# Optimization experiments

Measured on AMD Instinct MI355X. Metric: run time of the kernel, lower is better.

## Reference

```python
import jax, jax.numpy as jnp
import numpy as np

N, F, OUT = 8192, 256, 256


def setup_inputs() -> dict:
    key = jax.random.key(0)
    ks = jax.random.split(key, 8)
    s = 1.0 / np.sqrt(F)
    return {
        "features": jax.random.normal(ks[0], (N, F), jnp.float32),
        "key_features": jax.random.normal(ks[1], (N, F), jnp.float32),
        "adj_matrix": jax.random.uniform(ks[2], (N, N), jnp.float32),
        "W_d": jax.random.normal(ks[3], (2 * F, F), jnp.float32) * (1.0 / np.sqrt(2 * F)),
        "b_d": jnp.zeros((F,), jnp.float32),
        "W_o": jax.random.normal(ks[4], (F, OUT), jnp.float32) * s,
        "b_o": jnp.zeros((OUT,), jnp.float32),
        "W_a": jax.random.normal(ks[5], (F, F), jnp.float32) * s,
        "b_a": jnp.zeros((F,), jnp.float32),
        "W_ao": jax.random.normal(ks[6], (F, OUT), jnp.float32) * s,
        "b_ao": jnp.zeros((OUT,), jnp.float32),
    }


def reference(features, key_features, adj_matrix, W_d, b_d, W_o, b_o, W_a, b_a, W_ao, b_ao):
    n = features.shape[0]
    # masked softmax over rows; self-loop (diagonal) masked out
    neg = jnp.asarray(-1e9, adj_matrix.dtype)
    logits = adj_matrix * 5.0 + jnp.eye(n, dtype=adj_matrix.dtype) * neg
    a = jax.nn.softmax(logits, axis=-1)  # [N, N]
    # sum_j a_ij * concat(x_i, x_j) == concat(x_i * rowsum_i, (A @ X)_i)
    rowsum = jnp.sum(a, axis=-1, keepdims=True)  # == 1, kept for faithfulness
    agg = a @ features  # [N, F]
    neigh = jnp.concatenate([features * rowsum, agg], axis=-1)  # [N, 2F]
    neigh_distill = neigh @ W_d + b_d
    feature_updated = jnp.tanh((features - neigh_distill) @ W_o + b_o)
    # aggregate branch (withAgg=True)
    key_agg = (a @ key_features) @ W_a + b_a
    feature_aggregate = jnp.tanh((key_features + key_agg) @ W_ao + b_ao)
    return (feature_updated, feature_aggregate)
```

## Files before the change

### kernel.cpp

```cpp
#include <hip/hip_runtime.h>
#include <stdint.h>
#include <math.h>


typedef __attribute__((ext_vector_type(4)))  short bf16x4_t;
typedef __attribute__((ext_vector_type(8)))  short bf16x8_t;
typedef __attribute__((ext_vector_type(4)))  float f32x4_t;
typedef __attribute__((ext_vector_type(16))) float f32x16_t;

#define MFMA32(A, B, C) __builtin_amdgcn_mfma_f32_32x32x16_bf16(A, B, C, 0, 0, 0)
#define MFMA16(A, B, C) __builtin_amdgcn_mfma_f32_16x16x32_bf16(A, B, C, 0, 0, 0)

__device__ __forceinline__ unsigned short f2bf(float x) {
    union { float f; unsigned u; } c; c.f = x;
    unsigned u = c.u;
    return (unsigned short)((u + 0x7fffu + ((u >> 16) & 1u)) >> 16);
}
__device__ __forceinline__ unsigned pack2bf(float a, float b) {
    return (unsigned)f2bf(a) | ((unsigned)f2bf(b) << 16);
}
__device__ __forceinline__ float bflo(unsigned u) {
    union { unsigned u; float f; } c; c.u = u << 16; return c.f;
}
__device__ __forceinline__ float bfhi(unsigned u) {
    union { unsigned u; float f; } c; c.u = u & 0xffff0000u; return c.f;
}

__device__ __forceinline__ void gll16(const unsigned short* g, unsigned short* l) {
    __builtin_amdgcn_global_load_lds(
        (const __attribute__((address_space(1))) unsigned int*)(g),
        (__attribute__((address_space(3))) unsigned int*)(l), 16, 0, 0);
}

__global__ __launch_bounds__(256) void transpose_blob(
    const float* __restrict__ src, unsigned short* __restrict__ Xtb,
    unsigned* __restrict__ packdst, int c32base)
{
    __shared__ float tile[32][33];
    const int t = threadIdx.x;
    const int x = t & 31, y4 = (t >> 5) * 4;
    const int r0 = blockIdx.x * 32, c0 = blockIdx.y * 32;
#pragma unroll
    for (int i = 0; i < 4; ++i)
        tile[y4 + i][x] = src[(size_t)(r0 + y4 + i) * 256 + c0 + x];
    __syncthreads();
    const int s = t >> 7, lane = (t >> 1) & 63, e0 = (t & 1) * 4;
    const int kl = s * 16 + (lane >> 5) * 8 + e0;
    const int cl = lane & 31;
    unsigned short* blob = Xtb + ((size_t)blockIdx.x * 16 + (c0 >> 5) + c32base) * 1024;
    uint2 v;
    v.x = pack2bf(tile[kl][cl],     tile[kl + 1][cl]);
    v.y = pack2bf(tile[kl + 2][cl], tile[kl + 3][cl]);
    *(uint2*)(blob + t * 4) = v;
    const int prow = t >> 3, pc = t & 7;
    unsigned* pd = packdst + (size_t)(r0 + prow) * 256 + (c0 >> 1) + pc * 2;
    pd[0] = pack2bf(tile[prow][pc * 4 + 0], tile[prow][pc * 4 + 1]);
    pd[1] = pack2bf(tile[prow][pc * 4 + 2], tile[prow][pc * 4 + 3]);
}

__global__ __launch_bounds__(256) void compose1(
    const float* __restrict__ W_d, const float* __restrict__ W_o,
    const float* __restrict__ b_d, const float* __restrict__ b_o,
    unsigned short* __restrict__ W1t, float* __restrict__ c1)
{
    __shared__ float wrow[256];
    const int k = blockIdx.x, t = threadIdx.x;
    const float* srcrow = (k < 512) ? (W_d + (size_t)k * 256) : b_d;
    wrow[t] = srcrow[t];
    __syncthreads();
    float acc = 0.f;
#pragma unroll 8
    for (int m = 0; m < 256; ++m) acc = fmaf(wrow[m], W_o[(size_t)m * 256 + t], acc);
    if (k < 512)
        W1t[(size_t)t * 512 + k] = f2bf((k < 256 ? W_o[(size_t)k * 256 + t] : 0.f) - acc);
    else
        c1[t] = b_o[t] - acc;
}

__global__ __launch_bounds__(256) void compose2(
    const float* __restrict__ W_a, const float* __restrict__ W_ao,
    const float* __restrict__ b_a, const float* __restrict__ b_ao,
    unsigned short* __restrict__ W2t, float* __restrict__ c2)
{
    __shared__ float wrow[256];
    const int k = blockIdx.x, t = threadIdx.x;
    if (k < 256) {
        W2t[(size_t)t * 512 + k] = f2bf(W_ao[(size_t)k * 256 + t]);
        return;
    }
    const float* srcrow = (k < 512) ? (W_a + (size_t)(k - 256) * 256) : b_a;
    wrow[t] = srcrow[t];
    __syncthreads();
    float acc = 0.f;
#pragma unroll 8
    for (int m = 0; m < 256; ++m) acc = fmaf(wrow[m], W_ao[(size_t)m * 256 + t], acc);
    if (k < 512) W2t[(size_t)t * 512 + k] = f2bf(acc);
    else         c2[t] = b_ao[t] + acc;
}

#define ROWS 64
#define KSLICE 2048
#define NIT 64
#define NPH 32
#define ASTRIDE 36

struct QA { float4 v[2]; };

__global__ __launch_bounds__(512, 2) void exp_gemm(
    const float* __restrict__ adj, const unsigned short* __restrict__ Xtb,
    unsigned* __restrict__ UpartB, float* __restrict__ sSp)
{
    __shared__ unsigned short sA[2][2][ROWS * ASTRIDE];
    __shared__ uint4 sBq[8][4][256];
    unsigned short* const sB = (unsigned short*)sBq;

    const int t = threadIdx.x;
    const int w = t >> 6, lane = t & 63, q = lane >> 5, l31 = lane & 31;
    const int xcd = blockIdx.x & 7;
    const int h = xcd >> 1;
    const int rb = ((blockIdx.x >> 3) << 1) | (xcd & 1);
    const int row0 = rb * ROWS;
    const int kbase = h * KSLICE, jbase = h * (KSLICE / 32);

    const int srow = t >> 3, skoff = (t & 7) * 4;
    const int sgrow = row0 + srow;
    const float* adj_row = adj + (size_t)sgrow * 8192 + kbase + skoff;
    const int swoff = srow * ASTRIDE + skoff;

    const unsigned short* XtbW = Xtb + (size_t)jbase * 16384 + (size_t)(2 * w) * 1024 + lane * 8;
    unsigned short* const sBw = sB + (size_t)w * 4 * 2048;

    float rs = 0.f;
    f32x16_t acc[2][2];
#pragma unroll
    for (int mt = 0; mt < 2; ++mt)
#pragma unroll
        for (int ct = 0; ct < 2; ++ct)
#pragma unroll
            for (int e = 0; e < 16; ++e) acc[mt][ct][e] = 0.f;

    QA qa0, qa1, qa2, qa3;

    auto loadAdj = [&](int cidx, QA& qq) {
        qq.v[0] = *(const float4*)(adj_row + (size_t)(cidx * 2 + 0) * 32);
        qq.v[1] = *(const float4*)(adj_row + (size_t)(cidx * 2 + 1) * 32);
    };

    auto stageChunk = [&](int cidx, const QA& qq, int buf) {
#pragma unroll
        for (int ks = 0; ks < 2; ++ks) {
            const float4 v = qq.v[ks];
            float e0 = __expf(5.f * v.x);
            float e1 = __expf(5.f * v.y);
            float e2 = __expf(5.f * v.z);
            float e3 = __expf(5.f * v.w);
            const int gk = kbase + (cidx * 2 + ks) * 32 + skoff;
            if (gk + 0 == sgrow) e0 = 0.f;
            if (gk + 1 == sgrow) e1 = 0.f;
            if (gk + 2 == sgrow) e2 = 0.f;
            if (gk + 3 == sgrow) e3 = 0.f;
            rs += (e0 + e1) + (e2 + e3);
            uint2 p; p.x = pack2bf(e0, e1); p.y = pack2bf(e2, e3);
            *(uint2*)(&sA[buf][ks][swoff]) = p;
        }
    };

    auto issueB = [&](int jn, int slot) {
        const unsigned short* src = XtbW + (size_t)jn * 16384;
        unsigned short* dst = sBw + slot * 2048;
#pragma unroll
        for (int k4 = 0; k4 < 4; ++k4)
            gll16(src + k4 * 512, dst + k4 * 512);
    };

    auto consume = [&](int buf, int u, int slot) {
        const unsigned short* sa = &sA[buf][u][0] + l31 * ASTRIDE + q * 8;
        bf16x8_t af[2][2];
#pragma unroll
        for (int mt = 0; mt < 2; ++mt)
#pragma unroll
            for (int s = 0; s < 2; ++s) {
                const unsigned short* p = sa + mt * (32 * ASTRIDE) + s * 16;
                bf16x4_t lo = *(const bf16x4_t*)p;
                bf16x4_t hi = *(const bf16x4_t*)(p + 4);
                af[mt][s] = __builtin_shufflevector(lo, hi, 0, 1, 2, 3, 4, 5, 6, 7);
            }
        const unsigned short* sbp = sB + (size_t)(w * 4 + slot) * 2048 + lane * 8;
        bf16x8_t bfr[4];
#pragma unroll
        for (int k4 = 0; k4 < 4; ++k4)
            bfr[k4] = *(const bf16x8_t*)(sbp + k4 * 512);
        __builtin_amdgcn_s_setprio(1);
#pragma unroll
        for (int s = 0; s < 2; ++s)
#pragma unroll
            for (int mt = 0; mt < 2; ++mt)
#pragma unroll
                for (int ct = 0; ct < 2; ++ct)
                    acc[mt][ct] = MFMA32(af[mt][s], bfr[ct * 2 + s], acc[mt][ct]);
        __builtin_amdgcn_s_setprio(0);
    };

    auto phase = [&](int c, const QA& qstg, QA& qld, int buf) {
        if (c + 1 < NPH) stageChunk(c + 1, qstg, buf ^ 1);
        issueB((2 * c + 3) & 63, (2 * buf + 3) & 3);
        asm volatile("s_waitcnt vmcnt(16)" ::: "memory");
        consume(buf, 0, 2 * buf);
        issueB((2 * c + 4) & 63, 2 * buf);
        asm volatile("s_waitcnt vmcnt(14)" ::: "memory");
        consume(buf, 1, 2 * buf + 1);
        loadAdj((c + 4) & 31, qld);
        asm volatile("s_waitcnt lgkmcnt(0)\n\ts_barrier" ::: "memory");
    };

    issueB(0, 0); issueB(1, 1); issueB(2, 2);
    loadAdj(0, qa0); loadAdj(1, qa1); loadAdj(2, qa2); loadAdj(3, qa3);
    stageChunk(0, qa0, 0);
    asm volatile("s_waitcnt lgkmcnt(0)\n\ts_barrier" ::: "memory");

    for (int c0 = 0; c0 < NPH; c0 += 4) {
        phase(c0 + 0, qa1, qa0, 0);
        phase(c0 + 1, qa2, qa1, 1);
        phase(c0 + 2, qa3, qa2, 0);
        phase(c0 + 3, qa0, qa3, 1);
    }

    rs += __shfl_xor(rs, 1);
    rs += __shfl_xor(rs, 2);
    rs += __shfl_xor(rs, 4);
    if ((t & 7) == 0) sSp[h * 8192 + sgrow] = rs;

    unsigned* up = UpartB + (((size_t)h * 128 + rb) * 8 + w) * 2048 + lane;
#pragma unroll
    for (int mt = 0; mt < 2; ++mt)
#pragma unroll
        for (int ct = 0; ct < 2; ++ct)
#pragma unroll
            for (int ip = 0; ip < 8; ++ip)
                up[(size_t)(((mt * 2 + ct) * 8) + ip) * 64] =
                    pack2bf(acc[mt][ct][2 * ip], acc[mt][ct][2 * ip + 1]);
}

__global__ __launch_bounds__(256) void finalize_agg(
    const unsigned* __restrict__ UpartB, const float* __restrict__ sSp,
    unsigned* __restrict__ XcatN, unsigned* __restrict__ Kcat)
{
    __shared__ float sT[64][65];
    __shared__ float sInv[64];

    const int t = threadIdx.x;
    const int rb = blockIdx.x >> 3, wp = blockIdx.x & 7;
    const int row0 = rb * 64;

    if (t < 64) {
        const int r = row0 + t;
        sInv[t] = 1.f / (sSp[r] + sSp[8192 + r] + sSp[16384 + r] + sSp[24576 + r]);
    }

    const int i = t >> 3;
    const int l0 = (t & 7) * 8;
    const int mt = i >> 4, ct = (i >> 3) & 1, ip = i & 7;
    const int qq = l0 >> 5;
    const int rlo = mt * 32 + 2 * (ip & 1) + 8 * (ip >> 1) + 4 * qq;
    const int cbase = ct * 32 + (l0 & 31);

    float lo[8], hi[8];
#pragma unroll
    for (int j = 0; j < 8; ++j) { lo[j] = 0.f; hi[j] = 0.f; }
#pragma unroll
    for (int h = 0; h < 4; ++h) {
        const unsigned* src = UpartB + (((size_t)h * 128 + rb) * 8 + wp) * 2048
                              + (size_t)i * 64 + l0;
        const uint4 v0 = *(const uint4*)(src);
        const uint4 v1 = *(const uint4*)(src + 4);
        const unsigned vv[8] = { v0.x, v0.y, v0.z, v0.w, v1.x, v1.y, v1.z, v1.w };
#pragma unroll
        for (int j = 0; j < 8; ++j) { lo[j] += bflo(vv[j]); hi[j] += bfhi(vv[j]); }
    }
#pragma unroll
    for (int j = 0; j < 8; ++j) {
        sT[rlo][cbase + j]     = lo[j];
        sT[rlo + 1][cbase + j] = hi[j];
    }
    __syncthreads();

    const int row = t >> 2, cg = (t & 3) * 16;
    const float inv = sInv[row];
    unsigned outv[8];
#pragma unroll
    for (int j = 0; j < 8; ++j)
        outv[j] = pack2bf(sT[row][cg + 2 * j] * inv, sT[row][cg + 2 * j + 1] * inv);
    unsigned* dst = (wp < 4 ? XcatN : Kcat)
                    + (size_t)(row0 + row) * 256 + 128 + (wp & 3) * 32 + (cg >> 1);
    *(uint4*)(dst)     = *(const uint4*)(outv);
    *(uint4*)(dst + 4) = *(const uint4*)(outv + 4);
}

__global__ __launch_bounds__(256) void gemm_out(
    const unsigned short* __restrict__ Aa, const unsigned short* __restrict__ Wta,
    const float* __restrict__ ca,
    const unsigned short* __restrict__ Ab, const unsigned short* __restrict__ Wtb,
    const float* __restrict__ cb,
    float* __restrict__ outa, float* __restrict__ outb)
{
    __shared__ unsigned short sAm[32 * ASTRIDE];
    __shared__ unsigned short sB[256 * ASTRIDE];
    __shared__ float sBias[256];

    const int bid = blockIdx.x;
    const int prob = bid >> 8, tile = bid & 255;
    const unsigned short* A  = prob ? Ab  : Aa;
    const unsigned short* Wt = prob ? Wtb : Wta;
    const float* cvec        = prob ? cb  : ca;
    float* out               = prob ? outb : outa;

    const int t = threadIdx.x, w = t >> 6, lane = t & 63;
    const int m_lo = lane & 15, quad = lane >> 4;
    const int row0 = tile * 32;
    sBias[t] = cvec[t];

    f32x4_t acc[2][4];
#pragma unroll
    for (int a = 0; a < 2; ++a)
#pragma unroll
        for (int b = 0; b < 4; ++b)
#pragma unroll
            for (int e = 0; e < 4; ++e) acc[a][b][e] = 0.f;

    for (int ks = 0; ks < 16; ++ks) {
        const int k0 = ks * 32;
        __syncthreads();
        if (t < 128) {
            bf16x8_t v = *(const bf16x8_t*)(A + (size_t)(row0 + (t >> 2)) * 512 + k0 + (t & 3) * 8);
            unsigned short* d = &sAm[(t >> 2) * ASTRIDE + (t & 3) * 8];
            *(bf16x4_t*)d       = __builtin_shufflevector(v, v, 0, 1, 2, 3);
            *(bf16x4_t*)(d + 4) = __builtin_shufflevector(v, v, 4, 5, 6, 7);
        }
        {
            const unsigned short* src = Wt + (size_t)t * 512 + k0;
            unsigned short* d = &sB[t * ASTRIDE];
#pragma unroll
            for (int j = 0; j < 4; ++j) {
                bf16x8_t v = *(const bf16x8_t*)(src + j * 8);
                *(bf16x4_t*)(d + j * 8)     = __builtin_shufflevector(v, v, 0, 1, 2, 3);
                *(bf16x4_t*)(d + j * 8 + 4) = __builtin_shufflevector(v, v, 4, 5, 6, 7);
            }
        }
        __syncthreads();
        bf16x8_t a0, a1;
        {
            const unsigned short* p = &sAm[m_lo * ASTRIDE + quad * 8];
            bf16x4_t lo = *(const bf16x4_t*)p, hi = *(const bf16x4_t*)(p + 4);
            a0 = __builtin_shufflevector(lo, hi, 0, 1, 2, 3, 4, 5, 6, 7);
            p += 16 * ASTRIDE;
            lo = *(const bf16x4_t*)p; hi = *(const bf16x4_t*)(p + 4);
            a1 = __builtin_shufflevector(lo, hi, 0, 1, 2, 3, 4, 5, 6, 7);
        }
#pragma unroll
        for (int nt = 0; nt < 4; ++nt) {
            const unsigned short* p = &sB[(w * 64 + nt * 16 + m_lo) * ASTRIDE + quad * 8];
            bf16x4_t lo = *(const bf16x4_t*)p, hi = *(const bf16x4_t*)(p + 4);
            bf16x8_t b = __builtin_shufflevector(lo, hi, 0, 1, 2, 3, 4, 5, 6, 7);
            acc[0][nt] = MFMA16(a0, b, acc[0][nt]);
            acc[1][nt] = MFMA16(a1, b, acc[1][nt]);
        }
    }

#pragma unroll
    for (int mt = 0; mt < 2; ++mt)
#pragma unroll
        for (int nt = 0; nt < 4; ++nt) {
            const int col = w * 64 + nt * 16 + m_lo;
#pragma unroll
            for (int r = 0; r < 4; ++r) {
                const int row = row0 + mt * 16 + quad * 4 + r;
                out[(size_t)row * 256 + col] = tanhf(acc[mt][nt][r] + sBias[col]);
            }
        }
}

extern "C" void kernel_launch(void* const* d_in, const int* in_sizes, int n_in,
                              void* d_out, int out_size, void* d_ws, size_t ws_size,
                              hipStream_t stream) {
    const float* features = (const float*)d_in[0];
    const float* key      = (const float*)d_in[1];
    const float* adj      = (const float*)d_in[2];
    const float* W_d  = (const float*)d_in[3];
    const float* b_d  = (const float*)d_in[4];
    const float* W_o  = (const float*)d_in[5];
    const float* b_o  = (const float*)d_in[6];
    const float* W_a  = (const float*)d_in[7];
    const float* b_a  = (const float*)d_in[8];
    const float* W_ao = (const float*)d_in[9];
    const float* b_ao = (const float*)d_in[10];

    float* out1 = (float*)d_out;
    float* out2 = out1 + (size_t)8192 * 256;

    char* ws = (char*)d_ws;
    unsigned short* XcatN = (unsigned short*)(ws);
    unsigned short* Kcat  = (unsigned short*)(ws +  8388608);
    unsigned short* Xtb   = (unsigned short*)(ws + 16777216);
    unsigned*       UpartB= (unsigned*)      (ws + 25165824);
    float*          sSp   = (float*)         (ws + 58720256);
    unsigned short* W1t   = (unsigned short*)(ws + 58851328);
    unsigned short* W2t   = (unsigned short*)(ws + 59113472);
    float*          c1    = (float*)         (ws + 59375616);
    float*          c2    = (float*)         (ws + 59376640);

    dim3 blk(256);
    transpose_blob<<<dim3(256, 8), blk, 0, stream>>>(features, Xtb, (unsigned*)XcatN, 0);
    transpose_blob<<<dim3(256, 8), blk, 0, stream>>>(key, Xtb, (unsigned*)Kcat, 8);
    compose1<<<513, blk, 0, stream>>>(W_d, W_o, b_d, b_o, W1t, c1);
    compose2<<<513, blk, 0, stream>>>(W_a, W_ao, b_a, b_ao, W2t, c2);

    exp_gemm<<<512, dim3(512), 0, stream>>>(adj, Xtb, UpartB, sSp);
    finalize_agg<<<1024, blk, 0, stream>>>(UpartB, sSp,
                                           (unsigned*)XcatN, (unsigned*)Kcat);

    gemm_out<<<512, blk, 0, stream>>>(XcatN, W1t, c1, Kcat, W2t, c2, out1, out2);
}
```

Measured before the change: 516.4 us.

## Retile exp_gemm to 32-row blocks with 4 waves and per-wave B double buffering

Cuts the exp_gemm row tile from 64 to 32 rows and runs 256-thread blocks (1024 of them). Each wave now owns 128 output columns as four MFMA accumulators, and its B tiles sit in a two-slot LDS double buffer whose refill is issued right after the fragments are read. The exp is computed directly with exp2 and a folded constant, and finalize_agg is adapted to the new partial layout. The aim is more parallelism and simpler pipelining, at the cost of re-reading B from global memory for twice as many row blocks.

```diff
diff --git a/kernel.cpp b/kernel.cpp
--- a/kernel.cpp
+++ b/kernel.cpp
@@ -24,6 +24,9 @@
 }
 __device__ __forceinline__ float bfhi(unsigned u) {
     union { unsigned u; float f; } c; c.u = u & 0xffff0000u; return c.f;
+}
+__device__ __forceinline__ float exp5(float x) {
+    return __builtin_amdgcn_exp2f(7.2134752f * x);
 }
 
 __device__ __forceinline__ void gll16(const unsigned short* g, unsigned short* l) {
@@ -98,21 +101,19 @@
     else         c2[t] = b_ao[t] + acc;
 }
 
-#define ROWS 64
+#define ROWS 32
 #define KSLICE 2048
-#define NIT 64
 #define NPH 32
 #define ASTRIDE 36
 
 struct QA { float4 v[2]; };
 
-__global__ __launch_bounds__(512, 2) void exp_gemm(
+__global__ __launch_bounds__(256, 2) void exp_gemm(
     const float* __restrict__ adj, const unsigned short* __restrict__ Xtb,
     unsigned* __restrict__ UpartB, float* __restrict__ sSp)
 {
     __shared__ unsigned short sA[2][2][ROWS * ASTRIDE];
-    __shared__ uint4 sBq[8][4][256];
-    unsigned short* const sB = (unsigned short*)sBq;
+    __shared__ unsigned short sB[4][2][4096];
 
     const int t = threadIdx.x;
     const int w = t >> 6, lane = t & 63, q = lane >> 5, l31 = lane & 31;
@@ -127,17 +128,15 @@
     const float* adj_row = adj + (size_t)sgrow * 8192 + kbase + skoff;
     const int swoff = srow * ASTRIDE + skoff;
 
-    const unsigned short* XtbW = Xtb + (size_t)jbase * 16384 + (size_t)(2 * w) * 1024 + lane * 8;
-    unsigned short* const sBw = sB + (size_t)w * 4 * 2048;
+    const unsigned short* XtbW = Xtb + (size_t)jbase * 16384 + (size_t)w * 4096 + lane * 8;
+    unsigned short* const sBw = &sB[w][0][0];
 
     float rs = 0.f;
-    f32x16_t acc[2][2];
-#pragma unroll
-    for (int mt = 0; mt < 2; ++mt)
-#pragma unroll
-        for (int ct = 0; ct < 2; ++ct)
-#pragma unroll
-            for (int e = 0; e < 16; ++e) acc[mt][ct][e] = 0.f;
+    f32x16_t acc[4];
+#pragma unroll
+    for (int ct = 0; ct < 4; ++ct)
+#pragma unroll
+        for (int e = 0; e < 16; ++e) acc[ct][e] = 0.f;
 
     QA qa0, qa1, qa2, qa3;
 
@@ -150,10 +149,10 @@
 #pragma unroll
         for (int ks = 0; ks < 2; ++ks) {
             const float4 v = qq.v[ks];
-            float e0 = __expf(5.f * v.x);
-            float e1 = __expf(5.f * v.y);
-            float e2 = __expf(5.f * v.z);
-            float e3 = __expf(5.f * v.w);
+            float e0 = exp5(v.x);
+            float e1 = exp5(v.y);
+            float e2 = exp5(v.z);
+            float e3 = exp5(v.w);
             const int gk = kbase + (cidx * 2 + ks) * 32 + skoff;
             if (gk + 0 == sgrow) e0 = 0.f;
             if (gk + 1 == sgrow) e1 = 0.f;
@@ -167,53 +166,51 @@
 
     auto issueB = [&](int jn, int slot) {
         const unsigned short* src = XtbW + (size_t)jn * 16384;
-        unsigned short* dst = sBw + slot * 2048;
-#pragma unroll
-        for (int k4 = 0; k4 < 4; ++k4)
+        unsigned short* dst = sBw + slot * 4096;
+#pragma unroll
+        for (int k4 = 0; k4 < 8; ++k4)
             gll16(src + k4 * 512, dst + k4 * 512);
     };
 
-    auto consume = [&](int buf, int u, int slot) {
+    auto consume = [&](int buf, int u, int jnext) {
+        const unsigned short* sbp = sBw + u * 4096 + lane * 8;
+        bf16x8_t bfr[4][2];
+#pragma unroll
+        for (int ct = 0; ct < 4; ++ct)
+#pragma unroll
+            for (int s = 0; s < 2; ++s)
+                bfr[ct][s] = *(const bf16x8_t*)(sbp + ct * 1024 + s * 512);
         const unsigned short* sa = &sA[buf][u][0] + l31 * ASTRIDE + q * 8;
-        bf16x8_t af[2][2];
-#pragma unroll
-        for (int mt = 0; mt < 2; ++mt)
-#pragma unroll
-            for (int s = 0; s < 2; ++s) {
-                const unsigned short* p = sa + mt * (32 * ASTRIDE) + s * 16;
-                bf16x4_t lo = *(const bf16x4_t*)p;
-                bf16x4_t hi = *(const bf16x4_t*)(p + 4);
-                af[mt][s] = __builtin_shufflevector(lo, hi, 0, 1, 2, 3, 4, 5, 6, 7);
-            }
-        const unsigned short* sbp = sB + (size_t)(w * 4 + slot) * 2048 + lane * 8;
-        bf16x8_t bfr[4];
-#pragma unroll
-        for (int k4 = 0; k4 < 4; ++k4)
-            bfr[k4] = *(const bf16x8_t*)(sbp + k4 * 512);
+        bf16x8_t af[2];
+#pragma unroll
+        for (int s = 0; s < 2; ++s) {
+            const unsigned short* p = sa + s * 16;
+            bf16x4_t lo = *(const bf16x4_t*)p;
+            bf16x4_t hi = *(const bf16x4_t*)(p + 4);
+            af[s] = __builtin_shufflevector(lo, hi, 0, 1, 2, 3, 4, 5, 6, 7);
+        }
+        asm volatile("s_waitcnt lgkmcnt(0)" ::: "memory");
+        issueB(jnext, u);
         __builtin_amdgcn_s_setprio(1);
 #pragma unroll
         for (int s = 0; s < 2; ++s)
 #pragma unroll
-            for (int mt = 0; mt < 2; ++mt)
-#pragma unroll
-                for (int ct = 0; ct < 2; ++ct)
-                    acc[mt][ct] = MFMA32(af[mt][s], bfr[ct * 2 + s], acc[mt][ct]);
+            for (int ct = 0; ct < 4; ++ct)
+                acc[ct] = MFMA32(af[s], bfr[ct][s], acc[ct]);
         __builtin_amdgcn_s_setprio(0);
     };
 
     auto phase = [&](int c, const QA& qstg, QA& qld, int buf) {
         if (c + 1 < NPH) stageChunk(c + 1, qstg, buf ^ 1);
-        issueB((2 * c + 3) & 63, (2 * buf + 3) & 3);
-        asm volatile("s_waitcnt vmcnt(16)" ::: "memory");
-        consume(buf, 0, 2 * buf);
-        issueB((2 * c + 4) & 63, 2 * buf);
-        asm volatile("s_waitcnt vmcnt(14)" ::: "memory");
-        consume(buf, 1, 2 * buf + 1);
+        asm volatile("s_waitcnt vmcnt(10)" ::: "memory");
+        consume(buf, 0, (2 * c + 2) & 63);
+        asm volatile("s_waitcnt vmcnt(10)" ::: "memory");
+        consume(buf, 1, (2 * c + 3) & 63);
         loadAdj((c + 4) & 31, qld);
         asm volatile("s_waitcnt lgkmcnt(0)\n\ts_barrier" ::: "memory");
     };
 
-    issueB(0, 0); issueB(1, 1); issueB(2, 2);
+    issueB(0, 0); issueB(1, 1);
     loadAdj(0, qa0); loadAdj(1, qa1); loadAdj(2, qa2); loadAdj(3, qa3);
     stageChunk(0, qa0, 0);
     asm volatile("s_waitcnt lgkmcnt(0)\n\ts_barrier" ::: "memory");
@@ -230,70 +227,68 @@
     rs += __shfl_xor(rs, 4);
     if ((t & 7) == 0) sSp[h * 8192 + sgrow] = rs;
 
-    unsigned* up = UpartB + (((size_t)h * 128 + rb) * 8 + w) * 2048 + lane;
-#pragma unroll
-    for (int mt = 0; mt < 2; ++mt)
-#pragma unroll
-        for (int ct = 0; ct < 2; ++ct)
+    unsigned* upBase = UpartB + (((size_t)h * 256 + rb) * 8 + w * 2) * 1024 + lane;
+#pragma unroll
+    for (int cp = 0; cp < 2; ++cp)
+#pragma unroll
+        for (int c2 = 0; c2 < 2; ++c2)
 #pragma unroll
             for (int ip = 0; ip < 8; ++ip)
-                up[(size_t)(((mt * 2 + ct) * 8) + ip) * 64] =
-                    pack2bf(acc[mt][ct][2 * ip], acc[mt][ct][2 * ip + 1]);
+                upBase[(size_t)cp * 1024 + (c2 * 8 + ip) * 64] =
+                    pack2bf(acc[cp * 2 + c2][2 * ip], acc[cp * 2 + c2][2 * ip + 1]);
 }
 
 __global__ __launch_bounds__(256) void finalize_agg(
     const unsigned* __restrict__ UpartB, const float* __restrict__ sSp,
     unsigned* __restrict__ XcatN, unsigned* __restrict__ Kcat)
 {
-    __shared__ float sT[64][65];
-    __shared__ float sInv[64];
+    __shared__ float sT[32][65];
+    __shared__ float sInv[32];
 
     const int t = threadIdx.x;
     const int rb = blockIdx.x >> 3, wp = blockIdx.x & 7;
-    const int row0 = rb * 64;
-
-    if (t < 64) {
+    const int row0 = rb * 32;
+
+    if (t < 32) {
         const int r = row0 + t;
         sInv[t] = 1.f / (sSp[r] + sSp[8192 + r] + sSp[16384 + r] + sSp[24576 + r]);
     }
 
-    const int i = t >> 3;
-    const int l0 = (t & 7) * 8;
-    const int mt = i >> 4, ct = (i >> 3) & 1, ip = i & 7;
+    const int i = t >> 4;
+    const int l0 = (t & 15) * 4;
+    const int ct2 = i >> 3, ip = i & 7;
     const int qq = l0 >> 5;
-    const int rlo = mt * 32 + 2 * (ip & 1) + 8 * (ip >> 1) + 4 * qq;
-    const int cbase = ct * 32 + (l0 & 31);
-
-    float lo[8], hi[8];
-#pragma unroll
-    for (int j = 0; j < 8; ++j) { lo[j] = 0.f; hi[j] = 0.f; }
+    const int rlo = 2 * (ip & 1) + 8 * (ip >> 1) + 4 * qq;
+    const int cbase = ct2 * 32 + (l0 & 31);
+
+    float lo[4], hi[4];
+#pragma unroll
+    for (int j = 0; j < 4; ++j) { lo[j] = 0.f; hi[j] = 0.f; }
 #pragma unroll
     for (int h = 0; h < 4; ++h) {
-        const unsigned* src = UpartB + (((size_t)h * 128 + rb) * 8 + wp) * 2048
+        const unsigned* src = UpartB + (((size_t)h * 256 + rb) * 8 + wp) * 1024
                               + (size_t)i * 64 + l0;
         const uint4 v0 = *(const uint4*)(src);
-        const uint4 v1 = *(const uint4*)(src + 4);
-        const unsigned vv[8] = { v0.x, v0.y, v0.z, v0.w, v1.x, v1.y, v1.z, v1.w };
-#pragma unroll
-        for (int j = 0; j < 8; ++j) { lo[j] += bflo(vv[j]); hi[j] += bfhi(vv[j]); }
-    }
-#pragma unroll
-    for (int j = 0; j < 8; ++j) {
+        const unsigned vv[4] = { v0.x, v0.y, v0.z, v0.w };
+#pragma unroll
+        for (int j = 0; j < 4; ++j) { lo[j] += bflo(vv[j]); hi[j] += bfhi(vv[j]); }
+    }
+#pragma unroll
+    for (int j = 0; j < 4; ++j) {
         sT[rlo][cbase + j]     = lo[j];
         sT[rlo + 1][cbase + j] = hi[j];
     }
     __syncthreads();
 
-    const int row = t >> 2, cg = (t & 3) * 16;
+    const int row = t >> 3, cg = (t & 7) * 8;
     const float inv = sInv[row];
-    unsigned outv[8];
-#pragma unroll
-    for (int j = 0; j < 8; ++j)
+    unsigned outv[4];
+#pragma unroll
+    for (int j = 0; j < 4; ++j)
         outv[j] = pack2bf(sT[row][cg + 2 * j] * inv, sT[row][cg + 2 * j + 1] * inv);
     unsigned* dst = (wp < 4 ? XcatN : Kcat)
                     + (size_t)(row0 + row) * 256 + 128 + (wp & 3) * 32 + (cg >> 1);
-    *(uint4*)(dst)     = *(const uint4*)(outv);
-    *(uint4*)(dst + 4) = *(const uint4*)(outv + 4);
+    *(uint4*)(dst) = *(const uint4*)(outv);
 }
 
 __global__ __launch_bounds__(256) void gemm_out(
@@ -414,8 +409,8 @@
     compose1<<<513, blk, 0, stream>>>(W_d, W_o, b_d, b_o, W1t, c1);
     compose2<<<513, blk, 0, stream>>>(W_a, W_ao, b_a, b_ao, W2t, c2);
 
-    exp_gemm<<<512, dim3(512), 0, stream>>>(adj, Xtb, UpartB, sSp);
-    finalize_agg<<<1024, blk, 0, stream>>>(UpartB, sSp,
+    exp_gemm<<<1024, blk, 0, stream>>>(adj, Xtb, UpartB, sSp);
+    finalize_agg<<<2048, blk, 0, stream>>>(UpartB, sSp,
                                            (unsigned*)XcatN, (unsigned*)Kcat);
 
     gemm_out<<<512, blk, 0, stream>>>(XcatN, W1t, c1, Kcat, W2t, c2, out1, out2);
```

Result: slower. 531.0 us (+2.8%).

## Specialize exp_gemm waves into adj-exp producers and MFMA consumers

Applied to the files above, without the earlier changes.

Splits the 8 waves of exp_gemm into four producer waves that load adj, compute exp and stage bf16 tiles into LDS, and four consumer waves that stream X tiles and run MFMAs over wider column tiles (4 per wave instead of 2). The exp is also rewritten as a raw exp2 with a prescaled constant. The aim is to overlap the VALU-heavy exponent work with matrix-core work and cut per-wave B fragment traffic. finalize_agg is remapped to the new partial layout. The cost is that half the waves idle on MFMA, consumers hold larger accumulators, and the producer/consumer barrier coupling may stall.

```diff
diff --git a/kernel.cpp b/kernel.cpp
--- a/kernel.cpp
+++ b/kernel.cpp
@@ -24,6 +24,9 @@
 }
 __device__ __forceinline__ float bfhi(unsigned u) {
     union { unsigned u; float f; } c; c.u = u & 0xffff0000u; return c.f;
+}
+__device__ __forceinline__ float exp5(float x) {
+    return __builtin_amdgcn_exp2f(7.2134752f * x);
 }
 
 __device__ __forceinline__ void gll16(const unsigned short* g, unsigned short* l) {
@@ -99,20 +102,15 @@
 }
 
 #define ROWS 64
-#define KSLICE 2048
-#define NIT 64
 #define NPH 32
 #define ASTRIDE 36
-
-struct QA { float4 v[2]; };
 
 __global__ __launch_bounds__(512, 2) void exp_gemm(
     const float* __restrict__ adj, const unsigned short* __restrict__ Xtb,
     unsigned* __restrict__ UpartB, float* __restrict__ sSp)
 {
     __shared__ unsigned short sA[2][2][ROWS * ASTRIDE];
-    __shared__ uint4 sBq[8][4][256];
-    unsigned short* const sB = (unsigned short*)sBq;
+    __shared__ unsigned short sB[4][4][4096];
 
     const int t = threadIdx.x;
     const int w = t >> 6, lane = t & 63, q = lane >> 5, l31 = lane & 31;
@@ -120,125 +118,139 @@
     const int h = xcd >> 1;
     const int rb = ((blockIdx.x >> 3) << 1) | (xcd & 1);
     const int row0 = rb * ROWS;
-    const int kbase = h * KSLICE, jbase = h * (KSLICE / 32);
-
-    const int srow = t >> 3, skoff = (t & 7) * 4;
-    const int sgrow = row0 + srow;
-    const float* adj_row = adj + (size_t)sgrow * 8192 + kbase + skoff;
-    const int swoff = srow * ASTRIDE + skoff;
-
-    const unsigned short* XtbW = Xtb + (size_t)jbase * 16384 + (size_t)(2 * w) * 1024 + lane * 8;
-    unsigned short* const sBw = sB + (size_t)w * 4 * 2048;
-
-    float rs = 0.f;
-    f32x16_t acc[2][2];
-#pragma unroll
-    for (int mt = 0; mt < 2; ++mt)
-#pragma unroll
-        for (int ct = 0; ct < 2; ++ct)
-#pragma unroll
-            for (int e = 0; e < 16; ++e) acc[mt][ct][e] = 0.f;
-
-    QA qa0, qa1, qa2, qa3;
-
-    auto loadAdj = [&](int cidx, QA& qq) {
-        qq.v[0] = *(const float4*)(adj_row + (size_t)(cidx * 2 + 0) * 32);
-        qq.v[1] = *(const float4*)(adj_row + (size_t)(cidx * 2 + 1) * 32);
-    };
-
-    auto stageChunk = [&](int cidx, const QA& qq, int buf) {
-#pragma unroll
-        for (int ks = 0; ks < 2; ++ks) {
-            const float4 v = qq.v[ks];
-            float e0 = __expf(5.f * v.x);
-            float e1 = __expf(5.f * v.y);
-            float e2 = __expf(5.f * v.z);
-            float e3 = __expf(5.f * v.w);
-            const int gk = kbase + (cidx * 2 + ks) * 32 + skoff;
-            if (gk + 0 == sgrow) e0 = 0.f;
-            if (gk + 1 == sgrow) e1 = 0.f;
-            if (gk + 2 == sgrow) e2 = 0.f;
-            if (gk + 3 == sgrow) e3 = 0.f;
-            rs += (e0 + e1) + (e2 + e3);
-            uint2 p; p.x = pack2bf(e0, e1); p.y = pack2bf(e2, e3);
-            *(uint2*)(&sA[buf][ks][swoff]) = p;
-        }
-    };
-
-    auto issueB = [&](int jn, int slot) {
-        const unsigned short* src = XtbW + (size_t)jn * 16384;
-        unsigned short* dst = sBw + slot * 2048;
-#pragma unroll
-        for (int k4 = 0; k4 < 4; ++k4)
-            gll16(src + k4 * 512, dst + k4 * 512);
-    };
-
-    auto consume = [&](int buf, int u, int slot) {
-        const unsigned short* sa = &sA[buf][u][0] + l31 * ASTRIDE + q * 8;
-        bf16x8_t af[2][2];
+    const int kbase = h * 2048, jbase = h * 64;
+
+    if (__builtin_amdgcn_readfirstlane(w) < 4) {
+        const int srow = t >> 2;
+        const int skoff = (t & 3) * 8;
+        const int sgrow = row0 + srow;
+        const float* adj_row = adj + (size_t)sgrow * 8192 + kbase + skoff;
+        const int swoff = srow * ASTRIDE + skoff;
+        float rs = 0.f;
+        float4 qa[4][4];
+
+        auto loadAdj = [&](int cidx) {
+            float4* d = qa[cidx & 3];
+            const float* base = adj_row + (size_t)cidx * 64;
+            d[0] = *(const float4*)(base + 0);
+            d[1] = *(const float4*)(base + 4);
+            d[2] = *(const float4*)(base + 32);
+            d[3] = *(const float4*)(base + 36);
+        };
+        auto stageChunk = [&](int cidx, int buf) {
+            const float4* v = qa[cidx & 3];
+#pragma unroll
+            for (int ks = 0; ks < 2; ++ks) {
+                const float4 a = v[ks * 2], b = v[ks * 2 + 1];
+                float e[8];
+                e[0] = exp5(a.x); e[1] = exp5(a.y); e[2] = exp5(a.z); e[3] = exp5(a.w);
+                e[4] = exp5(b.x); e[5] = exp5(b.y); e[6] = exp5(b.z); e[7] = exp5(b.w);
+                const int gk = kbase + (cidx * 2 + ks) * 32 + skoff;
+#pragma unroll
+                for (int i = 0; i < 8; ++i)
+                    if (gk + i == sgrow) e[i] = 0.f;
+                rs += ((e[0] + e[1]) + (e[2] + e[3])) + ((e[4] + e[5]) + (e[6] + e[7]));
+                uint2 p0, p1;
+                p0.x = pack2bf(e[0], e[1]); p0.y = pack2bf(e[2], e[3]);
+                p1.x = pack2bf(e[4], e[5]); p1.y = pack2bf(e[6], e[7]);
+                *(uint2*)(&sA[buf][ks][swoff])     = p0;
+                *(uint2*)(&sA[buf][ks][swoff + 4]) = p1;
+            }
+        };
+
+        loadAdj(0); loadAdj(1); loadAdj(2); loadAdj(3);
+        asm volatile("s_waitcnt vmcnt(12)" ::: "memory");
+        stageChunk(0, 0);
+        asm volatile("s_waitcnt lgkmcnt(0)\n\ts_barrier" ::: "memory");
+
+        for (int c = 0; c < NPH; ++c) {
+            if (c + 1 < NPH) {
+                asm volatile("s_waitcnt vmcnt(8)" ::: "memory");
+                stageChunk(c + 1, (c + 1) & 1);
+            }
+            loadAdj((c + 4) & 31);
+            asm volatile("s_waitcnt lgkmcnt(0)\n\ts_barrier" ::: "memory");
+        }
+
+        rs += __shfl_xor(rs, 1);
+        rs += __shfl_xor(rs, 2);
+        if ((t & 3) == 0) sSp[h * 8192 + sgrow] = rs;
+    } else {
+        const int cw = w - 4;
+        const unsigned short* XtbW = Xtb + (size_t)jbase * 16384
+                                   + (size_t)cw * 4096 + lane * 8;
+        unsigned short* const sBw = &sB[cw][0][0];
+
+        f32x16_t acc[2][4];
 #pragma unroll
         for (int mt = 0; mt < 2; ++mt)
 #pragma unroll
-            for (int s = 0; s < 2; ++s) {
-                const unsigned short* p = sa + mt * (32 * ASTRIDE) + s * 16;
-                bf16x4_t lo = *(const bf16x4_t*)p;
-                bf16x4_t hi = *(const bf16x4_t*)(p + 4);
-                af[mt][s] = __builtin_shufflevector(lo, hi, 0, 1, 2, 3, 4, 5, 6, 7);
-            }
-        const unsigned short* sbp = sB + (size_t)(w * 4 + slot) * 2048 + lane * 8;
-        bf16x8_t bfr[4];
-#pragma unroll
-        for (int k4 = 0; k4 < 4; ++k4)
-            bfr[k4] = *(const bf16x8_t*)(sbp + k4 * 512);
-        __builtin_amdgcn_s_setprio(1);
-#pragma unroll
-        for (int s = 0; s < 2; ++s)
+            for (int ct = 0; ct < 4; ++ct)
+#pragma unroll
+                for (int e = 0; e < 16; ++e) acc[mt][ct][e] = 0.f;
+
+        auto issueB = [&](int jn, int slot) {
+            const unsigned short* src = XtbW + (size_t)jn * 16384;
+            unsigned short* dst = sBw + slot * 4096;
+#pragma unroll
+            for (int k4 = 0; k4 < 8; ++k4)
+                gll16(src + k4 * 512, dst + k4 * 512);
+        };
+        auto consume = [&](int buf, int u, int slot, int jnext) {
+            const unsigned short* sbp = sBw + slot * 4096 + lane * 8;
+            bf16x8_t bfr[4][2];
+#pragma unroll
+            for (int ct = 0; ct < 4; ++ct)
+#pragma unroll
+                for (int s = 0; s < 2; ++s)
+                    bfr[ct][s] = *(const bf16x8_t*)(sbp + ct * 1024 + s * 512);
+            const unsigned short* sa = &sA[buf][u][0] + l31 * ASTRIDE + q * 8;
+            bf16x8_t af[2][2];
 #pragma unroll
             for (int mt = 0; mt < 2; ++mt)
 #pragma unroll
-                for (int ct = 0; ct < 2; ++ct)
-                    acc[mt][ct] = MFMA32(af[mt][s], bfr[ct * 2 + s], acc[mt][ct]);
-        __builtin_amdgcn_s_setprio(0);
-    };
-
-    auto phase = [&](int c, const QA& qstg, QA& qld, int buf) {
-        if (c + 1 < NPH) stageChunk(c + 1, qstg, buf ^ 1);
-        issueB((2 * c + 3) & 63, (2 * buf + 3) & 3);
-        asm volatile("s_waitcnt vmcnt(16)" ::: "memory");
-        consume(buf, 0, 2 * buf);
-        issueB((2 * c + 4) & 63, 2 * buf);
-        asm volatile("s_waitcnt vmcnt(14)" ::: "memory");
-        consume(buf, 1, 2 * buf + 1);
-        loadAdj((c + 4) & 31, qld);
-        asm volatile("s_waitcnt lgkmcnt(0)\n\ts_barrier" ::: "memory");
-    };
-
-    issueB(0, 0); issueB(1, 1); issueB(2, 2);
-    loadAdj(0, qa0); loadAdj(1, qa1); loadAdj(2, qa2); loadAdj(3, qa3);
-    stageChunk(0, qa0, 0);
-    asm volatile("s_waitcnt lgkmcnt(0)\n\ts_barrier" ::: "memory");
-
-    for (int c0 = 0; c0 < NPH; c0 += 4) {
-        phase(c0 + 0, qa1, qa0, 0);
-        phase(c0 + 1, qa2, qa1, 1);
-        phase(c0 + 2, qa3, qa2, 0);
-        phase(c0 + 3, qa0, qa3, 1);
-    }
-
-    rs += __shfl_xor(rs, 1);
-    rs += __shfl_xor(rs, 2);
-    rs += __shfl_xor(rs, 4);
-    if ((t & 7) == 0) sSp[h * 8192 + sgrow] = rs;
-
-    unsigned* up = UpartB + (((size_t)h * 128 + rb) * 8 + w) * 2048 + lane;
-#pragma unroll
-    for (int mt = 0; mt < 2; ++mt)
-#pragma unroll
-        for (int ct = 0; ct < 2; ++ct)
-#pragma unroll
-            for (int ip = 0; ip < 8; ++ip)
-                up[(size_t)(((mt * 2 + ct) * 8) + ip) * 64] =
-                    pack2bf(acc[mt][ct][2 * ip], acc[mt][ct][2 * ip + 1]);
+                for (int s = 0; s < 2; ++s) {
+                    const unsigned short* p = sa + mt * (32 * ASTRIDE) + s * 16;
+                    bf16x4_t lo = *(const bf16x4_t*)p;
+                    bf16x4_t hi = *(const bf16x4_t*)(p + 4);
+                    af[mt][s] = __builtin_shufflevector(lo, hi, 0, 1, 2, 3, 4, 5, 6, 7);
+                }
+            asm volatile("s_waitcnt lgkmcnt(0)" ::: "memory");
+            issueB(jnext, slot);
+            __builtin_amdgcn_s_setprio(1);
+#pragma unroll
+            for (int s = 0; s < 2; ++s)
+#pragma unroll
+                for (int mt = 0; mt < 2; ++mt)
+#pragma unroll
+                    for (int ct = 0; ct < 4; ++ct)
+                        acc[mt][ct] = MFMA32(af[mt][s], bfr[ct][s], acc[mt][ct]);
+            __builtin_amdgcn_s_setprio(0);
+        };
+
+        issueB(0, 0); issueB(1, 1); issueB(2, 2); issueB(3, 3);
+        asm volatile("s_barrier" ::: "memory");
+
+        for (int c = 0; c < NPH; ++c) {
+            const int buf = c & 1;
+            const int j0 = 2 * c, j1 = 2 * c + 1;
+            asm volatile("s_waitcnt vmcnt(24)" ::: "memory");
+            consume(buf, 0, j0 & 3, (j0 + 4) & 63);
+            asm volatile("s_waitcnt vmcnt(24)" ::: "memory");
+            consume(buf, 1, j1 & 3, (j1 + 4) & 63);
+            asm volatile("s_waitcnt lgkmcnt(0)\n\ts_barrier" ::: "memory");
+        }
+
+        unsigned* up = UpartB + (((size_t)h * 128 + rb) * 4 + cw) * 4096 + lane;
+#pragma unroll
+        for (int mt = 0; mt < 2; ++mt)
+#pragma unroll
+            for (int ct = 0; ct < 4; ++ct)
+#pragma unroll
+                for (int ip = 0; ip < 8; ++ip)
+                    up[(size_t)(((mt * 4 + ct) * 8) + ip) * 64] =
+                        pack2bf(acc[mt][ct][2 * ip], acc[mt][ct][2 * ip + 1]);
+    }
 }
 
 __global__ __launch_bounds__(256) void finalize_agg(
@@ -249,7 +261,8 @@
     __shared__ float sInv[64];
 
     const int t = threadIdx.x;
-    const int rb = blockIdx.x >> 3, wp = blockIdx.x & 7;
+    const int rb = blockIdx.x >> 3, g = blockIdx.x & 7;
+    const int cw = g >> 1, hf = g & 1;
     const int row0 = rb * 64;
 
     if (t < 64) {
@@ -257,19 +270,19 @@
         sInv[t] = 1.f / (sSp[r] + sSp[8192 + r] + sSp[16384 + r] + sSp[24576 + r]);
     }
 
-    const int i = t >> 3;
+    const int mt = t >> 7, c2 = (t >> 6) & 1, ip = (t >> 3) & 7;
     const int l0 = (t & 7) * 8;
-    const int mt = i >> 4, ct = (i >> 3) & 1, ip = i & 7;
+    const int i = (mt * 4 + (2 * hf + c2)) * 8 + ip;
     const int qq = l0 >> 5;
     const int rlo = mt * 32 + 2 * (ip & 1) + 8 * (ip >> 1) + 4 * qq;
-    const int cbase = ct * 32 + (l0 & 31);
+    const int cbase = c2 * 32 + (l0 & 31);
 
     float lo[8], hi[8];
 #pragma unroll
     for (int j = 0; j < 8; ++j) { lo[j] = 0.f; hi[j] = 0.f; }
 #pragma unroll
     for (int h = 0; h < 4; ++h) {
-        const unsigned* src = UpartB + (((size_t)h * 128 + rb) * 8 + wp) * 2048
+        const unsigned* src = UpartB + (((size_t)h * 128 + rb) * 4 + cw) * 4096
                               + (size_t)i * 64 + l0;
         const uint4 v0 = *(const uint4*)(src);
         const uint4 v1 = *(const uint4*)(src + 4);
@@ -290,8 +303,8 @@
 #pragma unroll
     for (int j = 0; j < 8; ++j)
         outv[j] = pack2bf(sT[row][cg + 2 * j] * inv, sT[row][cg + 2 * j + 1] * inv);
-    unsigned* dst = (wp < 4 ? XcatN : Kcat)
-                    + (size_t)(row0 + row) * 256 + 128 + (wp & 3) * 32 + (cg >> 1);
+    unsigned* dst = (g < 4 ? XcatN : Kcat)
+                    + (size_t)(row0 + row) * 256 + 128 + (g & 3) * 32 + (cg >> 1);
     *(uint4*)(dst)     = *(const uint4*)(outv);
     *(uint4*)(dst + 4) = *(const uint4*)(outv + 4);
 }
```

New measurement: 584.0 us. 13.1% more time.
